# Kernel tuning notes

Measured on AMD Instinct MI355X. Metric: run time of the kernel, lower is better.

## Reference

```python
import jax, jax.numpy as jnp
import numpy as np

B, H, W, C = 32, 64, 64, 192
WS, SHIFT, NH = 8, 4, 6
HID = int(C * 2.0)
N = WS * WS
HD = C // NH
SCALE = HD ** -0.5


def _rel_index():
    coords = np.stack(np.meshgrid(np.arange(WS), np.arange(WS), indexing='ij')).reshape(2, -1)
    rel = (coords[:, :, None] - coords[:, None, :]).transpose(1, 2, 0)
    rel[:, :, 0] += WS - 1
    rel[:, :, 1] += WS - 1
    rel[:, :, 0] *= 2 * WS - 1
    return rel.sum(-1)  # [N, N] int


def _attn_mask():
    img = np.zeros((H, W))
    cnt = 0
    sl = (slice(0, -WS), slice(-WS, -SHIFT), slice(-SHIFT, None))
    for hs in sl:
        for ws_ in sl:
            img[hs, ws_] = cnt
            cnt += 1
    mw = img.reshape(H // WS, WS, W // WS, WS).transpose(0, 2, 1, 3).reshape(-1, N)
    am = mw[:, None, :] - mw[:, :, None]  # unsqueeze(1) - unsqueeze(2)
    return np.where(am != 0, -100.0, 0.0).astype(np.float32)  # [nW, N, N]

REL_IDX = jnp.asarray(_rel_index())
ATTN_MASK = jnp.asarray(_attn_mask())


def _ln(x, g, b, eps=1e-5):
    m = jnp.mean(x, -1, keepdims=True)
    v = jnp.mean((x - m) ** 2, -1, keepdims=True)
    return (x - m) * jax.lax.rsqrt(v + eps) * g + b


def setup_inputs() -> dict:
    key = jax.random.key(0)
    ks = jax.random.split(key, 16)
    s = 0.02
    return {
        'x': jax.random.normal(ks[0], (B, H, W, C), jnp.float32),
        'norm1_g': jnp.ones((C,), jnp.float32),
        'norm1_b': jnp.zeros((C,), jnp.float32),
        'qkv_w': jax.random.normal(ks[1], (C, 3 * C), jnp.float32) * s,
        'qkv_b': jnp.zeros((3 * C,), jnp.float32),
        'proj_w': jax.random.normal(ks[2], (C, C), jnp.float32) * s,
        'proj_b': jnp.zeros((C,), jnp.float32),
        'rel_bias_table': jax.random.normal(ks[3], ((2 * WS - 1) ** 2, NH), jnp.float32) * s,
        'norm2_g': jnp.ones((C,), jnp.float32),
        'norm2_b': jnp.zeros((C,), jnp.float32),
        'mlp_w1': jax.random.normal(ks[4], (C, HID), jnp.float32) * s,
        'mlp_b1': jnp.zeros((HID,), jnp.float32),
        'mlp_w2': jax.random.normal(ks[5], (HID, C), jnp.float32) * s,
        'mlp_b2': jnp.zeros((C,), jnp.float32),
    }


def reference(x, norm1_g, norm1_b, qkv_w, qkv_b, proj_w, proj_b, rel_bias_table,
              norm2_g, norm2_b, mlp_w1, mlp_b1, mlp_w2, mlp_b2):
    nWh, nWw = H // WS, W // WS
    nW = nWh * nWw
    shortcut = x
    h = _ln(x, norm1_g, norm1_b)
    # cyclic shift
    h = jnp.roll(h, shift=(-SHIFT, -SHIFT), axis=(1, 2))
    # window partition -> [B*nW, N, C]
    hw = h.reshape(B, nWh, WS, nWw, WS, C).transpose(0, 1, 3, 2, 4, 5).reshape(B * nW, N, C)
    # qkv
    qkv = hw @ qkv_w + qkv_b  # [B_, N, 3C]
    qkv = qkv.reshape(B * nW, N, 3, NH, HD).transpose(2, 0, 3, 1, 4)
    q, k, v = qkv[0], qkv[1], qkv[2]  # [B_, NH, N, HD]
    attn = jnp.einsum('bhnd,bhmd->bhnm', q * SCALE, k)
    # relative position bias: [NH, N, N]
    bias = rel_bias_table[REL_IDX.reshape(-1)].reshape(N, N, NH).transpose(2, 0, 1)
    attn = attn + bias[None]
    # shift mask
    attn = attn.reshape(B, nW, NH, N, N) + ATTN_MASK[None, :, None]
    attn = jax.nn.softmax(attn.reshape(B * nW, NH, N, N), axis=-1)
    out = jnp.einsum('bhnm,bhmd->bhnd', attn, v).transpose(0, 2, 1, 3).reshape(B * nW, N, C)
    out = out @ proj_w + proj_b
    # window reverse
    out = out.reshape(B, nWh, nWw, WS, WS, C).transpose(0, 1, 3, 2, 4, 5).reshape(B, H, W, C)
    out = jnp.roll(out, shift=(SHIFT, SHIFT), axis=(1, 2))
    h = shortcut + out
    # MLP
    m = _ln(h, norm2_g, norm2_b)
    m = jax.nn.gelu(m @ mlp_w1 + mlp_b1, approximate=False) @ mlp_w2 + mlp_b2
    return h + m
```

## Files before the change

### kernel.cpp

```cpp
#include <hip/hip_runtime.h>
#include <hip/hip_bf16.h>

#define CC 192

typedef __attribute__((ext_vector_type(8))) short bf16x8;
typedef __attribute__((ext_vector_type(4))) float f32x4;

__device__ __forceinline__ unsigned short f2bf(float f) {
    __hip_bfloat16 h = __float2bfloat16(f);
    unsigned short u;
    __builtin_memcpy(&u, &h, 2);
    return u;
}

__device__ __forceinline__ float bf2f(unsigned short u) {
    return __uint_as_float(((unsigned int)u) << 16);
}

__device__ __forceinline__ float fast_exp2(float x) {
#if __has_builtin(__builtin_amdgcn_exp2f)
    return __builtin_amdgcn_exp2f(x);
#else
    return __expf(0.69314718055994531f * x);
#endif
}

__device__ __forceinline__ f32x4 mfma16(bf16x8 a, bf16x8 b, f32x4 c) {
    return __builtin_amdgcn_mfma_f32_16x16x32_bf16(a, b, c, 0, 0, 0);
}

__global__ void k_prep(const float* __restrict__ qkv_w, const float* __restrict__ proj_w,
                       const float* __restrict__ w1, const float* __restrict__ w2,
                       const float* __restrict__ relTab,
                       unsigned short* __restrict__ qkvT, unsigned short* __restrict__ projT,
                       unsigned short* __restrict__ w1T, unsigned short* __restrict__ w2T,
                       unsigned short* __restrict__ biasT4) {
    int idx = blockIdx.x * blockDim.x + threadIdx.x;
    if (idx < 110592) { int n = idx / 192, k = idx % 192; qkvT[idx] = f2bf(qkv_w[k * 576 + n]); return; }
    idx -= 110592;
    if (idx < 36864)  { int n = idx / 192, k = idx % 192; projT[idx] = f2bf(proj_w[k * 192 + n]); return; }
    idx -= 36864;
    if (idx < 73728)  { int n = idx / 192, k = idx % 192; w1T[idx] = f2bf(w1[k * 384 + n]); return; }
    idx -= 73728;
    if (idx < 73728)  { int n = idx / 384, k = idx % 384; w2T[idx] = f2bf(w2[k * 192 + n]); return; }
    idx -= 73728;
    if (idx < 98304) {
        const int cls = idx / 24576, rem = idx % 24576;
        const int h = rem >> 12, i = (rem >> 6) & 63, j = rem & 63;
        const int yi = i >> 3, xi = i & 7, yj = j >> 3, xj = j & 7;
        const int rel = (yi - yj + 7) * 15 + (xi - xj + 7);
        float v = relTab[rel * 6 + h];
        const int bH = cls >> 1, bW = cls & 1;
        const int idi = (bH ? (yi >= 4 ? 2 : 1) : 0) * 3 + (bW ? (xi >= 4 ? 2 : 1) : 0);
        const int idj = (bH ? (yj >= 4 ? 2 : 1) : 0) * 3 + (bW ? (xj >= 4 ? 2 : 1) : 0);
        if (idi != idj) v -= 100.f;
        biasT4[idx] = f2bf(v * 1.4426950408889634f);
    }
}

__global__ __launch_bounds__(768, 3) void k_fused(
    const float* __restrict__ x,
    const float* __restrict__ n1g, const float* __restrict__ n1b,
    const unsigned short* __restrict__ qkvT, const float* __restrict__ qkv_b,
    const unsigned short* __restrict__ projT, const float* __restrict__ proj_b,
    const unsigned short* __restrict__ biasT4,
    const float* __restrict__ n2g, const float* __restrict__ n2b,
    const unsigned short* __restrict__ w1T, const float* __restrict__ b1,
    const unsigned short* __restrict__ w2T, const float* __restrict__ b2,
    float* __restrict__ out)
{
    __shared__ __align__(16) char smem[73728];
    __shared__ int sOpos[64];
    char* const rA = smem;
    char* const rQ = smem + 24576;
    char* const rK = smem + 49152;

    const int tid = threadIdx.x;
    const int wid = blockIdx.x;
    const int b = wid >> 6;
    const int win = wid & 63;
    const int wh = win >> 3, ww = win & 7;
    const int lane = tid & 63;
    const int wave = tid >> 6;
    const int lhi = lane >> 4, llo = lane & 15;

    if (tid < 512) {
        const int tok = tid >> 3;
        const int ch0 = (tid & 7) * 24;
        const int yi = tok >> 3, xi = tok & 7;
        const int oy = (wh * 8 + yi + 4) & 63;
        const int ox = (ww * 8 + xi + 4) & 63;
        const int base = ((b * 64 + oy) * 64 + ox) * CC;
        if ((tid & 7) == 0) sOpos[tok] = base;
        float v[24];
        float s = 0.f, ss = 0.f;
        #pragma unroll
        for (int i = 0; i < 6; ++i) {
            const float4 f = *(const float4*)(x + base + ch0 + i * 4);
            v[i*4+0]=f.x; v[i*4+1]=f.y; v[i*4+2]=f.z; v[i*4+3]=f.w;
            s  += f.x + f.y + f.z + f.w;
            ss += f.x*f.x + f.y*f.y + f.z*f.z + f.w*f.w;
        }
        s  += __shfl_xor(s, 1);  s  += __shfl_xor(s, 2);  s  += __shfl_xor(s, 4);
        ss += __shfl_xor(ss, 1); ss += __shfl_xor(ss, 2); ss += __shfl_xor(ss, 4);
        const float mean = s * (1.f / 192.f);
        const float rstd = rsqrtf(ss * (1.f / 192.f) - mean * mean + 1e-5f);
        char* aBase = rA + tok * 384;
        const int sw = (tok & 7) << 4;
        #pragma unroll
        for (int i = 0; i < 12; ++i) {
            const int c = ch0 + i * 2;
            const float a0 = (v[i*2+0] - mean) * rstd * n1g[c]   + n1b[c];
            const float a1 = (v[i*2+1] - mean) * rstd * n1g[c+1] + n1b[c+1];
            *(unsigned int*)(aBase + ((c * 2) ^ sw)) =
                (unsigned int)f2bf(a0) | ((unsigned int)f2bf(a1) << 16);
        }
    }
    bf16x8 pfQKV[3];
    #pragma unroll
    for (int n = 0; n < 3; ++n)
        pfQKV[n] = *(const bf16x8*)(qkvT + (wave * 48 + n * 16 + llo) * 192 + lhi * 8);
    __syncthreads();

    {
        const int cbase = wave * 48;
        f32x4 acc[4][3] = {};
        #pragma unroll
        for (int ks = 0; ks < 6; ++ks) {
            bf16x8 af[4];
            const int kbyte = ks * 64 + lhi * 16;
            #pragma unroll
            for (int m = 0; m < 4; ++m) {
                const int row = m * 16 + llo;
                af[m] = *(const bf16x8*)(rA + row * 384 + (kbyte ^ ((row & 7) << 4)));
            }
            #pragma unroll
            for (int n = 0; n < 3; ++n) {
                const bf16x8 bfr = (ks == 0) ? pfQKV[n]
                    : *(const bf16x8*)(qkvT + (cbase + n * 16 + llo) * 192 + ks * 32 + lhi * 8);
                #pragma unroll
                for (int m = 0; m < 4; ++m) acc[m][n] = mfma16(af[m], bfr, acc[m][n]);
            }
        }
        __syncthreads();
        #pragma unroll
        for (int n = 0; n < 3; ++n) {
            const int c0 = cbase + n * 16;
            const int which = c0 / 192;
            const int rem = c0 - which * 192;
            const int h = rem >> 5;
            const int d = (rem & 31) + llo;
            const float bia = qkv_b[c0 + llo];
            #pragma unroll
            for (int m = 0; m < 4; ++m) {
                #pragma unroll
                for (int r = 0; r < 4; ++r) {
                    const int row = m * 16 + lhi * 4 + r;
                    if (which == 0)
                        *(unsigned short*)(rQ + h * 4096 + row * 64 + ((2 * d) ^ ((row & 3) << 4)))
                            = f2bf((acc[m][n][r] + bia) * 0.2550510257216822f);
                    else if (which == 1)
                        *(unsigned short*)(rK + h * 4096 + row * 64 + ((2 * d) ^ ((row & 3) << 4)))
                            = f2bf(acc[m][n][r] + bia);
                    else
                        *(unsigned short*)(rA + h * 4096 + d * 128 + ((2 * row) ^ ((d & 7) << 4)))
                            = f2bf(acc[m][n][r] + bia);
                }
            }
        }
    }
    __syncthreads();

    const int h = wave >> 1;
    const int mh = wave & 1;
    f32x4 pacc[2][2] = {};
    float rinv[2][4];
    bf16x8 bfrP[6];
    {
        bf16x8 qf[2], kf[4];
        #pragma unroll
        for (int m = 0; m < 2; ++m) {
            const int t = (mh * 2 + m) * 16 + llo;
            qf[m] = *(const bf16x8*)(rQ + h * 4096 + t * 64 + ((lhi * 16) ^ ((t & 3) << 4)));
        }
        #pragma unroll
        for (int n = 0; n < 4; ++n) {
            const int t = n * 16 + llo;
            kf[n] = *(const bf16x8*)(rK + h * 4096 + t * 64 + ((lhi * 16) ^ ((t & 3) << 4)));
        }
        #pragma unroll
        for (int ks = 0; ks < 6; ++ks)
            bfrP[ks] = *(const bf16x8*)(projT + (wave * 16 + llo) * 192 + ks * 32 + lhi * 8);
        __syncthreads();

        f32x4 sacc[2][4] = {};
        #pragma unroll
        for (int m = 0; m < 2; ++m)
            #pragma unroll
            for (int n = 0; n < 4; ++n)
                sacc[m][n] = mfma16(qf[m], kf[n], sacc[m][n]);

        const int cls = ((wh == 7) ? 2 : 0) + ((ww == 7) ? 1 : 0);
        const unsigned short* bT = biasT4 + cls * 24576 + h * 4096;
        #pragma unroll
        for (int m = 0; m < 2; ++m) {
            #pragma unroll
            for (int r = 0; r < 4; ++r) {
                const int i = (mh * 2 + m) * 16 + lhi * 4 + r;
                float sum = 0.f;
                unsigned short pb[4];
                #pragma unroll
                for (int n = 0; n < 4; ++n) {
                    const int j = n * 16 + llo;
                    const float e = fast_exp2(sacc[m][n][r] + bf2f(bT[i * 64 + j]));
                    sum += e;
                    pb[n] = f2bf(e);
                }
                sum += __shfl_xor(sum, 1);
                sum += __shfl_xor(sum, 2);
                sum += __shfl_xor(sum, 4);
                sum += __shfl_xor(sum, 8);
                rinv[m][r] = 1.f / sum;
                #pragma unroll
                for (int n = 0; n < 4; ++n) {
                    const int j = n * 16 + llo;
                    *(unsigned short*)(rQ + h * 8192 + i * 128 + ((2 * j) ^ ((i & 7) << 4))) = pb[n];
                }
            }
        }
        #pragma unroll
        for (int ks = 0; ks < 2; ++ks) {
            bf16x8 pf[2];
            #pragma unroll
            for (int m = 0; m < 2; ++m) {
                const int t = (mh * 2 + m) * 16 + llo;
                pf[m] = *(const bf16x8*)(rQ + h * 8192 + t * 128 + ((ks * 64 + lhi * 16) ^ ((t & 7) << 4)));
            }
            #pragma unroll
            for (int n = 0; n < 2; ++n) {
                const int d = n * 16 + llo;
                const bf16x8 vf = *(const bf16x8*)(rA + h * 4096 + d * 128 + ((ks * 64 + lhi * 16) ^ ((d & 7) << 4)));
                #pragma unroll
                for (int m = 0; m < 2; ++m) pacc[m][n] = mfma16(pf[m], vf, pacc[m][n]);
            }
        }
    }
    __syncthreads();
    {
        #pragma unroll
        for (int m = 0; m < 2; ++m) {
            #pragma unroll
            for (int n = 0; n < 2; ++n) {
                const int c = h * 32 + n * 16 + llo;
                #pragma unroll
                for (int r = 0; r < 4; ++r) {
                    const int i = (mh * 2 + m) * 16 + lhi * 4 + r;
                    *(unsigned short*)(rA + i * 384 + ((c * 2) ^ ((i & 7) << 4)))
                        = f2bf(pacc[m][n][r] * rinv[m][r]);
                }
            }
        }
    }
    __syncthreads();

    bf16x8 bfrW1[6];
    {
        const int cbase = wave * 16;
        f32x4 acc[4] = {};
        #pragma unroll
        for (int ks = 0; ks < 6; ++ks) {
            bf16x8 af[4];
            const int kbyte = ks * 64 + lhi * 16;
            #pragma unroll
            for (int m = 0; m < 4; ++m) {
                const int row = m * 16 + llo;
                af[m] = *(const bf16x8*)(rA + row * 384 + (kbyte ^ ((row & 7) << 4)));
            }
            #pragma unroll
            for (int m = 0; m < 4; ++m) acc[m] = mfma16(af[m], bfrP[ks], acc[m]);
        }
        #pragma unroll
        for (int ks = 0; ks < 6; ++ks)
            bfrW1[ks] = *(const bf16x8*)(w1T + (wave * 16 + llo) * 192 + ks * 32 + lhi * 8);
        const int c = cbase + llo;
        const float pb = proj_b[c];
        #pragma unroll
        for (int m = 0; m < 4; ++m) {
            #pragma unroll
            for (int r = 0; r < 4; ++r) {
                const int i = m * 16 + lhi * 4 + r;
                const float hv = x[sOpos[i] + c] + acc[m][r] + pb;
                *(unsigned short*)(rQ + i * 384 + ((2 * c) ^ ((i & 7) << 4))) = f2bf(hv);
            }
        }
    }
    __syncthreads();

    if (tid < 512) {
        const int tok = tid >> 3;
        const int ch0 = (tid & 7) * 24;
        const int sw = (tok & 7) << 4;
        float v[24]; float s = 0.f, ss = 0.f;
        #pragma unroll
        for (int i = 0; i < 12; ++i) {
            const int c = ch0 + i * 2;
            const unsigned uu = *(const unsigned*)(rQ + tok * 384 + ((2 * c) ^ sw));
            const float a0 = bf2f((unsigned short)uu);
            const float a1 = bf2f((unsigned short)(uu >> 16));
            v[2*i] = a0; v[2*i+1] = a1;
            s += a0 + a1;
            ss += a0 * a0 + a1 * a1;
        }
        s  += __shfl_xor(s, 1);  s  += __shfl_xor(s, 2);  s  += __shfl_xor(s, 4);
        ss += __shfl_xor(ss, 1); ss += __shfl_xor(ss, 2); ss += __shfl_xor(ss, 4);
        const float mean = s * (1.f / 192.f);
        const float rstd = rsqrtf(ss * (1.f / 192.f) - mean * mean + 1e-5f);
        char* aBase = rA + tok * 384;
        #pragma unroll
        for (int i = 0; i < 12; ++i) {
            const int c = ch0 + i * 2;
            const float a0 = (v[i*2]   - mean) * rstd * n2g[c]   + n2b[c];
            const float a1 = (v[i*2+1] - mean) * rstd * n2g[c+1] + n2b[c+1];
            *(unsigned int*)(aBase + ((c * 2) ^ sw)) =
                (unsigned int)f2bf(a0) | ((unsigned int)f2bf(a1) << 16);
        }
    }
    __syncthreads();

    f32x4 accM[4] = {};
    #pragma unroll
    for (int hh = 0; hh < 2; ++hh) {
        {
            f32x4 a1[4] = {};
            #pragma unroll
            for (int ks = 0; ks < 6; ++ks) {
                bf16x8 af[4];
                const int kbyte = ks * 64 + lhi * 16;
                #pragma unroll
                for (int m = 0; m < 4; ++m) {
                    const int row = m * 16 + llo;
                    af[m] = *(const bf16x8*)(rA + row * 384 + (kbyte ^ ((row & 7) << 4)));
                }
                const bf16x8 bfr = (hh == 0) ? bfrW1[ks]
                    : *(const bf16x8*)(w1T + (192 + wave * 16 + llo) * 192 + ks * 32 + lhi * 8);
                #pragma unroll
                for (int m = 0; m < 4; ++m) a1[m] = mfma16(af[m], bfr, a1[m]);
            }
            const int cl = wave * 16 + llo;
            const float bb = b1[hh * 192 + cl];
            #pragma unroll
            for (int m = 0; m < 4; ++m) {
                #pragma unroll
                for (int r = 0; r < 4; ++r) {
                    const int i = m * 16 + lhi * 4 + r;
                    const float u = a1[m][r] + bb;
                    const float xx = 2.3022211096534824f * (u + 0.044715f * u * u * u);
                    const float g = u / (1.f + fast_exp2(-xx));
                    *(unsigned short*)(rK + i * 384 + ((2 * cl) ^ ((i & 7) << 4))) = f2bf(g);
                }
            }
        }
        __syncthreads();
        {
            #pragma unroll
            for (int ks = 0; ks < 6; ++ks) {
                bf16x8 af[4];
                const int kbyte = ks * 64 + lhi * 16;
                #pragma unroll
                for (int m = 0; m < 4; ++m) {
                    const int row = m * 16 + llo;
                    af[m] = *(const bf16x8*)(rK + row * 384 + (kbyte ^ ((row & 7) << 4)));
                }
                const bf16x8 bfr = *(const bf16x8*)(w2T + (wave * 16 + llo) * 384 + hh * 192 + ks * 32 + lhi * 8);
                #pragma unroll
                for (int m = 0; m < 4; ++m) accM[m] = mfma16(af[m], bfr, accM[m]);
            }
        }
        if (hh == 0) __syncthreads();
    }
    {
        const int c = wave * 16 + llo;
        const float bb = b2[c];
        #pragma unroll
        for (int m = 0; m < 4; ++m) {
            #pragma unroll
            for (int r = 0; r < 4; ++r) {
                const int i = m * 16 + lhi * 4 + r;
                const float hv = bf2f(*(const unsigned short*)(rQ + i * 384 + ((2 * c) ^ ((i & 7) << 4))));
                out[sOpos[i] + c] = hv + accM[m][r] + bb;
            }
        }
    }
}

extern "C" void kernel_launch(void* const* d_in, const int* in_sizes, int n_in,
                              void* d_out, int out_size, void* d_ws, size_t ws_size,
                              hipStream_t stream)
{
    const float* x      = (const float*)d_in[0];
    const float* n1g    = (const float*)d_in[1];
    const float* n1b    = (const float*)d_in[2];
    const float* qkv_w  = (const float*)d_in[3];
    const float* qkv_b  = (const float*)d_in[4];
    const float* proj_w = (const float*)d_in[5];
    const float* proj_b = (const float*)d_in[6];
    const float* relTab = (const float*)d_in[7];
    const float* n2g    = (const float*)d_in[8];
    const float* n2b    = (const float*)d_in[9];
    const float* w1     = (const float*)d_in[10];
    const float* b1     = (const float*)d_in[11];
    const float* w2     = (const float*)d_in[12];
    const float* b2     = (const float*)d_in[13];
    float* out = (float*)d_out;

    char* ws = (char*)d_ws;
    unsigned short* qkvT   = (unsigned short*)(ws);
    unsigned short* projT  = (unsigned short*)(ws + 221184);
    unsigned short* w1T    = (unsigned short*)(ws + 294912);
    unsigned short* w2T    = (unsigned short*)(ws + 442368);
    unsigned short* biasT4 = (unsigned short*)(ws + 589824);

    k_prep<<<1536, 256, 0, stream>>>(qkv_w, proj_w, w1, w2, relTab, qkvT, projT, w1T, w2T, biasT4);
    k_fused<<<2048, 768, 0, stream>>>(x, n1g, n1b, qkvT, qkv_b, projT, proj_b, biasT4,
                                      n2g, n2b, w1T, b1, w2T, b2, out);
}
```

Measured before the change: 281.0 us.

## Process two windows per workgroup to reuse weight fragments across 128 tokens

Each workgroup of the fused Swin block now handles two shifted windows (128 tokens) instead of one, and the grid is halved. Every weight fragment loaded from global memory (QKV, proj, MLP W1/W2) now feeds twice as many MFMAs, and attention gives each of the 12 waves one (window, head) pair. The cost is doubled LDS use (about 147 KB), which likely allows only one workgroup per CU, plus larger accumulator register arrays. That reduces the latency hiding that a second resident block used to provide.

Result: faster. 262.0 us, median of 2 (-6.7%).

```diff
diff --git a/kernel.cpp b/kernel.cpp
--- a/kernel.cpp
+++ b/kernel.cpp
@@ -69,35 +69,35 @@
     const unsigned short* __restrict__ w2T, const float* __restrict__ b2,
     float* __restrict__ out)
 {
-    __shared__ __align__(16) char smem[73728];
-    __shared__ int sOpos[64];
+    __shared__ __align__(16) char smem[147456];
+    __shared__ int sOpos[128];
     char* const rA = smem;
-    char* const rQ = smem + 24576;
-    char* const rK = smem + 49152;
+    char* const rQ = smem + 49152;
+    char* const rK = smem + 98304;
 
     const int tid = threadIdx.x;
     const int wid = blockIdx.x;
-    const int b = wid >> 6;
-    const int win = wid & 63;
-    const int wh = win >> 3, ww = win & 7;
     const int lane = tid & 63;
     const int wave = tid >> 6;
     const int lhi = lane >> 4, llo = lane & 15;
 
-    if (tid < 512) {
-        const int tok = tid >> 3;
+    auto ln1_token = [&](int t) {
+        const int v = t >> 6;
+        const int gwin = wid * 2 + v;
+        const int bb_ = gwin >> 6;
+        const int win_ = gwin & 63;
+        const int tok = t & 63;
+        const int oy = ((win_ >> 3) * 8 + (tok >> 3) + 4) & 63;
+        const int ox = ((win_ & 7) * 8 + (tok & 7) + 4) & 63;
+        const int base = ((bb_ * 64 + oy) * 64 + ox) * CC;
         const int ch0 = (tid & 7) * 24;
-        const int yi = tok >> 3, xi = tok & 7;
-        const int oy = (wh * 8 + yi + 4) & 63;
-        const int ox = (ww * 8 + xi + 4) & 63;
-        const int base = ((b * 64 + oy) * 64 + ox) * CC;
-        if ((tid & 7) == 0) sOpos[tok] = base;
-        float v[24];
+        if ((tid & 7) == 0) sOpos[t] = base;
+        float vv[24];
         float s = 0.f, ss = 0.f;
         #pragma unroll
         for (int i = 0; i < 6; ++i) {
             const float4 f = *(const float4*)(x + base + ch0 + i * 4);
-            v[i*4+0]=f.x; v[i*4+1]=f.y; v[i*4+2]=f.z; v[i*4+3]=f.w;
+            vv[i*4+0]=f.x; vv[i*4+1]=f.y; vv[i*4+2]=f.z; vv[i*4+3]=f.w;
             s  += f.x + f.y + f.z + f.w;
             ss += f.x*f.x + f.y*f.y + f.z*f.z + f.w*f.w;
         }
@@ -105,209 +105,212 @@
         ss += __shfl_xor(ss, 1); ss += __shfl_xor(ss, 2); ss += __shfl_xor(ss, 4);
         const float mean = s * (1.f / 192.f);
         const float rstd = rsqrtf(ss * (1.f / 192.f) - mean * mean + 1e-5f);
-        char* aBase = rA + tok * 384;
-        const int sw = (tok & 7) << 4;
+        char* aBase = rA + t * 384;
+        const int sw = (t & 7) << 4;
         #pragma unroll
         for (int i = 0; i < 12; ++i) {
             const int c = ch0 + i * 2;
-            const float a0 = (v[i*2+0] - mean) * rstd * n1g[c]   + n1b[c];
-            const float a1 = (v[i*2+1] - mean) * rstd * n1g[c+1] + n1b[c+1];
+            const float a0 = (vv[i*2+0] - mean) * rstd * n1g[c]   + n1b[c];
+            const float a1 = (vv[i*2+1] - mean) * rstd * n1g[c+1] + n1b[c+1];
             *(unsigned int*)(aBase + ((c * 2) ^ sw)) =
                 (unsigned int)f2bf(a0) | ((unsigned int)f2bf(a1) << 16);
         }
-    }
-    bf16x8 pfQKV[3];
-    #pragma unroll
-    for (int n = 0; n < 3; ++n)
-        pfQKV[n] = *(const bf16x8*)(qkvT + (wave * 48 + n * 16 + llo) * 192 + lhi * 8);
+    };
+    ln1_token(tid >> 3);
+    if (tid < 256) ln1_token(96 + (tid >> 3));
     __syncthreads();
 
     {
         const int cbase = wave * 48;
-        f32x4 acc[4][3] = {};
+        f32x4 acc[2][4][3] = {};
         #pragma unroll
         for (int ks = 0; ks < 6; ++ks) {
-            bf16x8 af[4];
             const int kbyte = ks * 64 + lhi * 16;
-            #pragma unroll
-            for (int m = 0; m < 4; ++m) {
-                const int row = m * 16 + llo;
-                af[m] = *(const bf16x8*)(rA + row * 384 + (kbyte ^ ((row & 7) << 4)));
-            }
+            bf16x8 bfr[3];
+            #pragma unroll
+            for (int n = 0; n < 3; ++n)
+                bfr[n] = *(const bf16x8*)(qkvT + (cbase + n * 16 + llo) * 192 + ks * 32 + lhi * 8);
+            #pragma unroll
+            for (int v = 0; v < 2; ++v) {
+                bf16x8 af[4];
+                #pragma unroll
+                for (int m = 0; m < 4; ++m) {
+                    const int row = v * 64 + m * 16 + llo;
+                    af[m] = *(const bf16x8*)(rA + row * 384 + (kbyte ^ ((row & 7) << 4)));
+                }
+                #pragma unroll
+                for (int n = 0; n < 3; ++n)
+                    #pragma unroll
+                    for (int m = 0; m < 4; ++m)
+                        acc[v][m][n] = mfma16(af[m], bfr[n], acc[v][m][n]);
+            }
+        }
+        __syncthreads();
+        #pragma unroll
+        for (int v = 0; v < 2; ++v) {
             #pragma unroll
             for (int n = 0; n < 3; ++n) {
-                const bf16x8 bfr = (ks == 0) ? pfQKV[n]
-                    : *(const bf16x8*)(qkvT + (cbase + n * 16 + llo) * 192 + ks * 32 + lhi * 8);
-                #pragma unroll
-                for (int m = 0; m < 4; ++m) acc[m][n] = mfma16(af[m], bfr, acc[m][n]);
-            }
-        }
-        __syncthreads();
-        #pragma unroll
-        for (int n = 0; n < 3; ++n) {
-            const int c0 = cbase + n * 16;
-            const int which = c0 / 192;
-            const int rem = c0 - which * 192;
-            const int h = rem >> 5;
-            const int d = (rem & 31) + llo;
-            const float bia = qkv_b[c0 + llo];
-            #pragma unroll
-            for (int m = 0; m < 4; ++m) {
-                #pragma unroll
-                for (int r = 0; r < 4; ++r) {
-                    const int row = m * 16 + lhi * 4 + r;
-                    if (which == 0)
-                        *(unsigned short*)(rQ + h * 4096 + row * 64 + ((2 * d) ^ ((row & 3) << 4)))
-                            = f2bf((acc[m][n][r] + bia) * 0.2550510257216822f);
-                    else if (which == 1)
-                        *(unsigned short*)(rK + h * 4096 + row * 64 + ((2 * d) ^ ((row & 3) << 4)))
-                            = f2bf(acc[m][n][r] + bia);
-                    else
-                        *(unsigned short*)(rA + h * 4096 + d * 128 + ((2 * row) ^ ((d & 7) << 4)))
-                            = f2bf(acc[m][n][r] + bia);
-                }
-            }
-        }
-    }
-    __syncthreads();
-
-    const int h = wave >> 1;
-    const int mh = wave & 1;
-    f32x4 pacc[2][2] = {};
-    float rinv[2][4];
-    bf16x8 bfrP[6];
+                const int c0 = cbase + n * 16;
+                const int which = c0 / 192;
+                const int rem = c0 - which * 192;
+                const int hs = v * 6 + (rem >> 5);
+                const int d = (rem & 31) + llo;
+                const float bia = qkv_b[c0 + llo];
+                #pragma unroll
+                for (int m = 0; m < 4; ++m) {
+                    #pragma unroll
+                    for (int r = 0; r < 4; ++r) {
+                        const int row = m * 16 + lhi * 4 + r;
+                        if (which == 0)
+                            *(unsigned short*)(rQ + hs * 4096 + row * 64 + ((2 * d) ^ ((row & 3) << 4)))
+                                = f2bf((acc[v][m][n][r] + bia) * 0.2550510257216822f);
+                        else if (which == 1)
+                            *(unsigned short*)(rK + hs * 4096 + row * 64 + ((2 * d) ^ ((row & 3) << 4)))
+                                = f2bf(acc[v][m][n][r] + bia);
+                        else
+                            *(unsigned short*)(rA + hs * 4096 + d * 128 + ((2 * row) ^ ((d & 7) << 4)))
+                                = f2bf(acc[v][m][n][r] + bia);
+                    }
+                }
+            }
+        }
+    }
+    __syncthreads();
+
+    const int v = wave / 6;
+    const int h = wave - v * 6;
+    const int hs = wave;
+    f32x4 pacc[2][2][2] = {};
+    float rinv[2][2][4];
     {
-        bf16x8 qf[2], kf[4];
-        #pragma unroll
-        for (int m = 0; m < 2; ++m) {
-            const int t = (mh * 2 + m) * 16 + llo;
-            qf[m] = *(const bf16x8*)(rQ + h * 4096 + t * 64 + ((lhi * 16) ^ ((t & 3) << 4)));
+        bf16x8 qf[4], kf[4];
+        #pragma unroll
+        for (int m = 0; m < 4; ++m) {
+            const int t = m * 16 + llo;
+            qf[m] = *(const bf16x8*)(rQ + hs * 4096 + t * 64 + ((lhi * 16) ^ ((t & 3) << 4)));
         }
         #pragma unroll
         for (int n = 0; n < 4; ++n) {
             const int t = n * 16 + llo;
-            kf[n] = *(const bf16x8*)(rK + h * 4096 + t * 64 + ((lhi * 16) ^ ((t & 3) << 4)));
-        }
-        #pragma unroll
-        for (int ks = 0; ks < 6; ++ks)
-            bfrP[ks] = *(const bf16x8*)(projT + (wave * 16 + llo) * 192 + ks * 32 + lhi * 8);
+            kf[n] = *(const bf16x8*)(rK + hs * 4096 + t * 64 + ((lhi * 16) ^ ((t & 3) << 4)));
+        }
         __syncthreads();
 
-        f32x4 sacc[2][4] = {};
-        #pragma unroll
-        for (int m = 0; m < 2; ++m)
-            #pragma unroll
-            for (int n = 0; n < 4; ++n)
-                sacc[m][n] = mfma16(qf[m], kf[n], sacc[m][n]);
-
-        const int cls = ((wh == 7) ? 2 : 0) + ((ww == 7) ? 1 : 0);
+        const int win_ = (wid * 2 + v) & 63;
+        const int cls = (((win_ >> 3) == 7) ? 2 : 0) + (((win_ & 7) == 7) ? 1 : 0);
         const unsigned short* bT = biasT4 + cls * 24576 + h * 4096;
-        #pragma unroll
-        for (int m = 0; m < 2; ++m) {
+        char* const pBase = rQ + hs * 8192;
+        #pragma unroll
+        for (int hh = 0; hh < 2; ++hh) {
+            f32x4 sacc[2][4] = {};
+            #pragma unroll
+            for (int m = 0; m < 2; ++m)
+                #pragma unroll
+                for (int n = 0; n < 4; ++n)
+                    sacc[m][n] = mfma16(qf[hh * 2 + m], kf[n], sacc[m][n]);
+            #pragma unroll
+            for (int m = 0; m < 2; ++m) {
+                #pragma unroll
+                for (int r = 0; r < 4; ++r) {
+                    const int i = (hh * 2 + m) * 16 + lhi * 4 + r;
+                    float sum = 0.f;
+                    unsigned short pb[4];
+                    #pragma unroll
+                    for (int n = 0; n < 4; ++n) {
+                        const int j = n * 16 + llo;
+                        const float e = fast_exp2(sacc[m][n][r] + bf2f(bT[i * 64 + j]));
+                        sum += e;
+                        pb[n] = f2bf(e);
+                    }
+                    sum += __shfl_xor(sum, 1);
+                    sum += __shfl_xor(sum, 2);
+                    sum += __shfl_xor(sum, 4);
+                    sum += __shfl_xor(sum, 8);
+                    rinv[hh][m][r] = 1.f / sum;
+                    #pragma unroll
+                    for (int n = 0; n < 4; ++n) {
+                        const int j = n * 16 + llo;
+                        *(unsigned short*)(pBase + i * 128 + ((2 * j) ^ ((i & 7) << 4))) = pb[n];
+                    }
+                }
+            }
+            #pragma unroll
+            for (int ks = 0; ks < 2; ++ks) {
+                bf16x8 pf[2];
+                #pragma unroll
+                for (int m = 0; m < 2; ++m) {
+                    const int t = (hh * 2 + m) * 16 + llo;
+                    pf[m] = *(const bf16x8*)(pBase + t * 128 + ((ks * 64 + lhi * 16) ^ ((t & 7) << 4)));
+                }
+                #pragma unroll
+                for (int n = 0; n < 2; ++n) {
+                    const int d = n * 16 + llo;
+                    const bf16x8 vf = *(const bf16x8*)(rA + hs * 4096 + d * 128 + ((ks * 64 + lhi * 16) ^ ((d & 7) << 4)));
+                    #pragma unroll
+                    for (int m = 0; m < 2; ++m) pacc[hh][m][n] = mfma16(pf[m], vf, pacc[hh][m][n]);
+                }
+            }
+        }
+    }
+    __syncthreads();
+    {
+        #pragma unroll
+        for (int hh = 0; hh < 2; ++hh) {
+            #pragma unroll
+            for (int m = 0; m < 2; ++m) {
+                #pragma unroll
+                for (int n = 0; n < 2; ++n) {
+                    const int c = h * 32 + n * 16 + llo;
+                    #pragma unroll
+                    for (int r = 0; r < 4; ++r) {
+                        const int t = v * 64 + (hh * 2 + m) * 16 + lhi * 4 + r;
+                        *(unsigned short*)(rA + t * 384 + ((c * 2) ^ ((t & 7) << 4)))
+                            = f2bf(pacc[hh][m][n][r] * rinv[hh][m][r]);
+                    }
+                }
+            }
+        }
+    }
+    __syncthreads();
+
+    {
+        const int c = wave * 16 + llo;
+        f32x4 acc[8] = {};
+        #pragma unroll
+        for (int ks = 0; ks < 6; ++ks) {
+            const int kbyte = ks * 64 + lhi * 16;
+            const bf16x8 bfr = *(const bf16x8*)(projT + c * 192 + ks * 32 + lhi * 8);
+            #pragma unroll
+            for (int m = 0; m < 8; ++m) {
+                const int row = m * 16 + llo;
+                const bf16x8 af = *(const bf16x8*)(rA + row * 384 + (kbyte ^ ((row & 7) << 4)));
+                acc[m] = mfma16(af, bfr, acc[m]);
+            }
+        }
+        const float pb = proj_b[c];
+        #pragma unroll
+        for (int m = 0; m < 8; ++m) {
             #pragma unroll
             for (int r = 0; r < 4; ++r) {
-                const int i = (mh * 2 + m) * 16 + lhi * 4 + r;
-                float sum = 0.f;
-                unsigned short pb[4];
-                #pragma unroll
-                for (int n = 0; n < 4; ++n) {
-                    const int j = n * 16 + llo;
-                    const float e = fast_exp2(sacc[m][n][r] + bf2f(bT[i * 64 + j]));
-                    sum += e;
-                    pb[n] = f2bf(e);
-                }
-                sum += __shfl_xor(sum, 1);
-                sum += __shfl_xor(sum, 2);
-                sum += __shfl_xor(sum, 4);
-                sum += __shfl_xor(sum, 8);
-                rinv[m][r] = 1.f / sum;
-                #pragma unroll
-                for (int n = 0; n < 4; ++n) {
-                    const int j = n * 16 + llo;
-                    *(unsigned short*)(rQ + h * 8192 + i * 128 + ((2 * j) ^ ((i & 7) << 4))) = pb[n];
-                }
-            }
-        }
-        #pragma unroll
-        for (int ks = 0; ks < 2; ++ks) {
-            bf16x8 pf[2];
-            #pragma unroll
-            for (int m = 0; m < 2; ++m) {
-                const int t = (mh * 2 + m) * 16 + llo;
-                pf[m] = *(const bf16x8*)(rQ + h * 8192 + t * 128 + ((ks * 64 + lhi * 16) ^ ((t & 7) << 4)));
-            }
-            #pragma unroll
-            for (int n = 0; n < 2; ++n) {
-                const int d = n * 16 + llo;
-                const bf16x8 vf = *(const bf16x8*)(rA + h * 4096 + d * 128 + ((ks * 64 + lhi * 16) ^ ((d & 7) << 4)));
-                #pragma unroll
-                for (int m = 0; m < 2; ++m) pacc[m][n] = mfma16(pf[m], vf, pacc[m][n]);
-            }
-        }
-    }
-    __syncthreads();
-    {
-        #pragma unroll
-        for (int m = 0; m < 2; ++m) {
-            #pragma unroll
-            for (int n = 0; n < 2; ++n) {
-                const int c = h * 32 + n * 16 + llo;
-                #pragma unroll
-                for (int r = 0; r < 4; ++r) {
-                    const int i = (mh * 2 + m) * 16 + lhi * 4 + r;
-                    *(unsigned short*)(rA + i * 384 + ((c * 2) ^ ((i & 7) << 4)))
-                        = f2bf(pacc[m][n][r] * rinv[m][r]);
-                }
-            }
-        }
-    }
-    __syncthreads();
-
-    bf16x8 bfrW1[6];
-    {
-        const int cbase = wave * 16;
-        f32x4 acc[4] = {};
-        #pragma unroll
-        for (int ks = 0; ks < 6; ++ks) {
-            bf16x8 af[4];
-            const int kbyte = ks * 64 + lhi * 16;
-            #pragma unroll
-            for (int m = 0; m < 4; ++m) {
-                const int row = m * 16 + llo;
-                af[m] = *(const bf16x8*)(rA + row * 384 + (kbyte ^ ((row & 7) << 4)));
-            }
-            #pragma unroll
-            for (int m = 0; m < 4; ++m) acc[m] = mfma16(af[m], bfrP[ks], acc[m]);
-        }
-        #pragma unroll
-        for (int ks = 0; ks < 6; ++ks)
-            bfrW1[ks] = *(const bf16x8*)(w1T + (wave * 16 + llo) * 192 + ks * 32 + lhi * 8);
-        const int c = cbase + llo;
-        const float pb = proj_b[c];
-        #pragma unroll
-        for (int m = 0; m < 4; ++m) {
-            #pragma unroll
-            for (int r = 0; r < 4; ++r) {
-                const int i = m * 16 + lhi * 4 + r;
-                const float hv = x[sOpos[i] + c] + acc[m][r] + pb;
-                *(unsigned short*)(rQ + i * 384 + ((2 * c) ^ ((i & 7) << 4))) = f2bf(hv);
-            }
-        }
-    }
-    __syncthreads();
-
-    if (tid < 512) {
-        const int tok = tid >> 3;
+                const int t = m * 16 + lhi * 4 + r;
+                const float hv = x[sOpos[t] + c] + acc[m][r] + pb;
+                *(unsigned short*)(rQ + t * 384 + ((2 * c) ^ ((t & 7) << 4))) = f2bf(hv);
+            }
+        }
+    }
+    __syncthreads();
+
+    auto ln2_token = [&](int t) {
         const int ch0 = (tid & 7) * 24;
-        const int sw = (tok & 7) << 4;
-        float v[24]; float s = 0.f, ss = 0.f;
+        const int sw = (t & 7) << 4;
+        float vv[24]; float s = 0.f, ss = 0.f;
         #pragma unroll
         for (int i = 0; i < 12; ++i) {
             const int c = ch0 + i * 2;
-            const unsigned uu = *(const unsigned*)(rQ + tok * 384 + ((2 * c) ^ sw));
+            const unsigned uu = *(const unsigned*)(rQ + t * 384 + ((2 * c) ^ sw));
             const float a0 = bf2f((unsigned short)uu);
             const float a1 = bf2f((unsigned short)(uu >> 16));
-            v[2*i] = a0; v[2*i+1] = a1;
+            vv[2*i] = a0; vv[2*i+1] = a1;
             s += a0 + a1;
             ss += a0 * a0 + a1 * a1;
         }
@@ -315,65 +318,63 @@
         ss += __shfl_xor(ss, 1); ss += __shfl_xor(ss, 2); ss += __shfl_xor(ss, 4);
         const float mean = s * (1.f / 192.f);
         const float rstd = rsqrtf(ss * (1.f / 192.f) - mean * mean + 1e-5f);
-        char* aBase = rA + tok * 384;
+        char* aBase = rA + t * 384;
         #pragma unroll
         for (int i = 0; i < 12; ++i) {
             const int c = ch0 + i * 2;
-            const float a0 = (v[i*2]   - mean) * rstd * n2g[c]   + n2b[c];
-            const float a1 = (v[i*2+1] - mean) * rstd * n2g[c+1] + n2b[c+1];
+            const float a0 = (vv[i*2]   - mean) * rstd * n2g[c]   + n2b[c];
+            const float a1 = (vv[i*2+1] - mean) * rstd * n2g[c+1] + n2b[c+1];
             *(unsigned int*)(aBase + ((c * 2) ^ sw)) =
                 (unsigned int)f2bf(a0) | ((unsigned int)f2bf(a1) << 16);
         }
-    }
-    __syncthreads();
-
-    f32x4 accM[4] = {};
+    };
+    ln2_token(tid >> 3);
+    if (tid < 256) ln2_token(96 + (tid >> 3));
+    __syncthreads();
+
+    f32x4 accM[8] = {};
     #pragma unroll
     for (int hh = 0; hh < 2; ++hh) {
         {
-            f32x4 a1[4] = {};
+            const int cl = wave * 16 + llo;
+            f32x4 a1[8] = {};
             #pragma unroll
             for (int ks = 0; ks < 6; ++ks) {
-                bf16x8 af[4];
                 const int kbyte = ks * 64 + lhi * 16;
-                #pragma unroll
-                for (int m = 0; m < 4; ++m) {
+                const bf16x8 bfr = *(const bf16x8*)(w1T + (hh * 192 + cl) * 192 + ks * 32 + lhi * 8);
+                #pragma unroll
+                for (int m = 0; m < 8; ++m) {
                     const int row = m * 16 + llo;
-                    af[m] = *(const bf16x8*)(rA + row * 384 + (kbyte ^ ((row & 7) << 4)));
-                }
-                const bf16x8 bfr = (hh == 0) ? bfrW1[ks]
-                    : *(const bf16x8*)(w1T + (192 + wave * 16 + llo) * 192 + ks * 32 + lhi * 8);
-                #pragma unroll
-                for (int m = 0; m < 4; ++m) a1[m] = mfma16(af[m], bfr, a1[m]);
-            }
-            const int cl = wave * 16 + llo;
+                    const bf16x8 af = *(const bf16x8*)(rA + row * 384 + (kbyte ^ ((row & 7) << 4)));
+                    a1[m] = mfma16(af, bfr, a1[m]);
+                }
+            }
             const float bb = b1[hh * 192 + cl];
             #pragma unroll
-            for (int m = 0; m < 4; ++m) {
+            for (int m = 0; m < 8; ++m) {
                 #pragma unroll
                 for (int r = 0; r < 4; ++r) {
-                    const int i = m * 16 + lhi * 4 + r;
+                    const int t = m * 16 + lhi * 4 + r;
                     const float u = a1[m][r] + bb;
                     const float xx = 2.3022211096534824f * (u + 0.044715f * u * u * u);
                     const float g = u / (1.f + fast_exp2(-xx));
-                    *(unsigned short*)(rK + i * 384 + ((2 * cl) ^ ((i & 7) << 4))) = f2bf(g);
+                    *(unsigned short*)(rK + t * 384 + ((2 * cl) ^ ((t & 7) << 4))) = f2bf(g);
                 }
             }
         }
         __syncthreads();
         {
+            const int c = wave * 16 + llo;
             #pragma unroll
             for (int ks = 0; ks < 6; ++ks) {
-                bf16x8 af[4];
                 const int kbyte = ks * 64 + lhi * 16;
-                #pragma unroll
-                for (int m = 0; m < 4; ++m) {
+                const bf16x8 bfr = *(const bf16x8*)(w2T + c * 384 + hh * 192 + ks * 32 + lhi * 8);
+                #pragma unroll
+                for (int m = 0; m < 8; ++m) {
                     const int row = m * 16 + llo;
-                    af[m] = *(const bf16x8*)(rK + row * 384 + (kbyte ^ ((row & 7) << 4)));
-                }
-                const bf16x8 bfr = *(const bf16x8*)(w2T + (wave * 16 + llo) * 384 + hh * 192 + ks * 32 + lhi * 8);
-                #pragma unroll
-                for (int m = 0; m < 4; ++m) accM[m] = mfma16(af[m], bfr, accM[m]);
+                    const bf16x8 af = *(const bf16x8*)(rK + row * 384 + (kbyte ^ ((row & 7) << 4)));
+                    accM[m] = mfma16(af, bfr, accM[m]);
+                }
             }
         }
         if (hh == 0) __syncthreads();
@@ -382,12 +383,12 @@
         const int c = wave * 16 + llo;
         const float bb = b2[c];
         #pragma unroll
-        for (int m = 0; m < 4; ++m) {
+        for (int m = 0; m < 8; ++m) {
             #pragma unroll
             for (int r = 0; r < 4; ++r) {
-                const int i = m * 16 + lhi * 4 + r;
-                const float hv = bf2f(*(const unsigned short*)(rQ + i * 384 + ((2 * c) ^ ((i & 7) << 4))));
-                out[sOpos[i] + c] = hv + accM[m][r] + bb;
+                const int t = m * 16 + lhi * 4 + r;
+                const float hv = bf2f(*(const unsigned short*)(rQ + t * 384 + ((2 * c) ^ ((t & 7) << 4))));
+                out[sOpos[t] + c] = hv + accM[m][r] + bb;
             }
         }
     }
@@ -421,6 +422,6 @@
     unsigned short* biasT4 = (unsigned short*)(ws + 589824);
 
     k_prep<<<1536, 256, 0, stream>>>(qkv_w, proj_w, w1, w2, relTab, qkvT, projT, w1T, w2T, biasT4);
-    k_fused<<<2048, 768, 0, stream>>>(x, n1g, n1b, qkvT, qkv_b, projT, proj_b, biasT4,
+    k_fused<<<1024, 768, 0, stream>>>(x, n1g, n1b, qkvT, qkv_b, projT, proj_b, biasT4,
                                       n2g, n2b, w1T, b1, w2T, b2, out);
 }
```
